# Optimization experiments

Hardware: AMD Instinct MI355X
Metric: run time of the kernel (lower is better)

Reference implementation:

```python
import jax, jax.numpy as jnp
import numpy as np

NUM_HEADS = 16
EMBED_DIM = 1024
HEAD_DIM = EMBED_DIM // NUM_HEADS  # 64
BS, L = 2, 4096


def setup_inputs() -> dict:
    key = jax.random.key(0)
    ks = jax.random.split(key, 11)
    s = 1.0 / np.sqrt(EMBED_DIM)
    inp = {
        "x": jax.random.normal(ks[0], (BS, L, EMBED_DIM), dtype=jnp.float32),
        "mask": jax.random.randint(ks[1], (1, 1, L, L), 0, 2, dtype=jnp.int32),
        # weights stored as [in, out] so y = x @ W + b (math-equivalent to nn.Linear)
        "Wq": jax.random.uniform(ks[2], (EMBED_DIM, EMBED_DIM), jnp.float32, -s, s),
        "bq": jax.random.uniform(ks[3], (EMBED_DIM,), jnp.float32, -s, s),
        "Wk": jax.random.uniform(ks[4], (EMBED_DIM, EMBED_DIM), jnp.float32, -s, s),
        "bk": jax.random.uniform(ks[5], (EMBED_DIM,), jnp.float32, -s, s),
        "Wv": jax.random.uniform(ks[6], (EMBED_DIM, EMBED_DIM), jnp.float32, -s, s),
        "bv": jax.random.uniform(ks[7], (EMBED_DIM,), jnp.float32, -s, s),
        "Wo": jax.random.uniform(ks[8], (EMBED_DIM, EMBED_DIM), jnp.float32, -s, s),
        "bo": jax.random.uniform(ks[9], (EMBED_DIM,), jnp.float32, -s, s),
    }
    return inp


def reference(x, mask, Wq, bq, Wk, bk, Wv, bv, Wo, bo):
    bs, length, _ = x.shape
    scale = jnp.asarray(HEAD_DIM ** 0.5, x.dtype)

    def split_heads(t):  # [b, l, d] -> [b, h, l, hd]
        return t.reshape(bs, length, NUM_HEADS, HEAD_DIM).transpose(0, 2, 1, 3)

    q = split_heads(x @ Wq + bq)
    k = split_heads(x @ Wk + bk)
    v = split_heads(x @ Wv + bv)

    # scores: [b, h, lq, lk]
    scores = jnp.einsum("bhqd,bhkd->bhqk", q, k) / scale
    scores = scores + mask.astype(x.dtype) * jnp.asarray(-10000.0, x.dtype)
    attn = jax.nn.softmax(scores, axis=-1)  # dropout p=0 -> identity

    out = jnp.einsum("bhqk,bhkd->bhqd", attn, v)  # [b, h, l, hd]
    out = out.transpose(0, 2, 1, 3).reshape(bs, length, EMBED_DIM)
    return out @ Wo + bo
```

## Files before the change

### kernel.cpp

```cpp
#include <hip/hip_runtime.h>
#include <stdint.h>

#define SEQ_LEN 4096
#define N_HEADS 16
#define H_DIM 64
#define E_DIM 1024
#define NBH 32
#define M_TOT 8192

typedef __attribute__((ext_vector_type(8))) short short8;
typedef __attribute__((ext_vector_type(4))) short s16x4;
typedef __attribute__((ext_vector_type(4))) float f32x4;
typedef __attribute__((ext_vector_type(4))) unsigned short u16x4;

__device__ __forceinline__ unsigned short f2bf(float f) {
  union { float f; uint32_t u; } c; c.f = f;
  uint32_t u = c.u;
  u += 0x7FFFu + ((u >> 16) & 1u);
  return (unsigned short)(u >> 16);
}

__device__ __forceinline__ f32x4 mfma16(short8 a, short8 b, f32x4 c) {
  return __builtin_amdgcn_mfma_f32_16x16x32_bf16(a, b, c, 0, 0, 0);
}

__device__ __forceinline__ uint32_t cvtpk_bf16(float a, float b) {
  uint32_t r;
  asm("v_cvt_pk_bf16_f32 %0, %1, %2" : "=v"(r) : "v"(a), "v"(b));
  return r;
}

__device__ __forceinline__ float bperm_f(int srcLane, float v) {
  union { float f; int i; } c; c.f = v;
  c.i = __builtin_amdgcn_ds_bpermute(srcLane << 2, c.i);
  return c.f;
}


__global__ __launch_bounds__(256) void cast_x_kernel(const float* __restrict__ x,
                                                     unsigned short* __restrict__ xb) {
  const int i = (blockIdx.x * 256 + threadIdx.x) * 4;
  const f32x4 v = *(const f32x4*)(x + i);
  u16x4 o;
  #pragma unroll
  for (int j = 0; j < 4; j++) o[j] = f2bf(v[j]);
  *(u16x4*)(xb + i) = o;
}

__global__ __launch_bounds__(256) void transpose_w_kernel(
    const float* __restrict__ Wq, const float* __restrict__ Wk,
    const float* __restrict__ Wv, const float* __restrict__ Wo,
    unsigned short* __restrict__ Wqkvt, unsigned short* __restrict__ Wot) {
  __shared__ float tile[32][33];
  const int z = blockIdx.z;
  const float* src = (z == 0) ? Wq : (z == 1) ? Wk : (z == 2) ? Wv : Wo;
  unsigned short* dst = (z < 3) ? (Wqkvt + (size_t)z * E_DIM * E_DIM) : Wot;
  const int n0 = blockIdx.x * 32, k0 = blockIdx.y * 32;
  const int tx = threadIdx.x, ty = threadIdx.y;
  #pragma unroll
  for (int i = 0; i < 4; i++)
    tile[ty + i * 8][tx] = src[(size_t)(k0 + ty + i * 8) * E_DIM + n0 + tx];
  __syncthreads();
  #pragma unroll
  for (int i = 0; i < 4; i++)
    dst[(size_t)(n0 + ty + i * 8) * E_DIM + k0 + tx] = f2bf(tile[tx][ty + i * 8]);
}

__global__ __launch_bounds__(256) void pack_mask_kernel(const int* __restrict__ mask,
                                                        unsigned long long* __restrict__ mw) {
  const int e = blockIdx.x * 256 + threadIdx.x;
  const int bit = mask[e] != 0;
  const unsigned long long bal = __ballot(bit);
  if ((threadIdx.x & 63) == 0) mw[e >> 6] = bal;
}

#define LDT 40
#define QSCALE 0.18033688011112042f

template<int MODE>
__global__ __launch_bounds__(256) void gemm_kernel(
    const unsigned short* __restrict__ A,
    const unsigned short* __restrict__ Bt,
    const float* __restrict__ b0, const float* __restrict__ b1, const float* __restrict__ b2,
    unsigned short* __restrict__ Qo, unsigned short* __restrict__ Ko,
    unsigned short* __restrict__ Vto, float* __restrict__ Co)
{
  __shared__ unsigned short As[128 * LDT];
  __shared__ unsigned short Bs[128 * LDT];
  const int tid = threadIdx.x;
  const int lane = tid & 63, wid = tid >> 6;
  const int l15 = lane & 15, g = lane >> 4;
  const int bm = blockIdx.x * 128, bn = blockIdx.y * 128;
  const int wm = (wid >> 1) * 64, wn = (wid & 1) * 64;

  const int srow = tid >> 2, scol = (tid & 3) * 8;
  const unsigned short* ap0 = A  + (size_t)(bm + srow) * E_DIM + scol;
  const unsigned short* ap1 = ap0 + (size_t)64 * E_DIM;
  const unsigned short* bp0 = Bt + (size_t)(bn + srow) * E_DIM + scol;
  const unsigned short* bp1 = bp0 + (size_t)64 * E_DIM;
  unsigned short* aw0 = As + srow * LDT + scol;
  unsigned short* aw1 = aw0 + 64 * LDT;
  unsigned short* bw0 = Bs + srow * LDT + scol;
  unsigned short* bw1 = bw0 + 64 * LDT;

  f32x4 acc[4][4] = {};

  for (int k0 = 0; k0 < E_DIM; k0 += 32) {
    const short8 ra0 = *(const short8*)(ap0 + k0);
    const short8 ra1 = *(const short8*)(ap1 + k0);
    const short8 rb0 = *(const short8*)(bp0 + k0);
    const short8 rb1 = *(const short8*)(bp1 + k0);
    __syncthreads();
    *(short8*)aw0 = ra0;  *(short8*)aw1 = ra1;
    *(short8*)bw0 = rb0;  *(short8*)bw1 = rb1;
    __syncthreads();
    short8 af[4], bf[4];
    #pragma unroll
    for (int i = 0; i < 4; i++)
      af[i] = *(const short8*)(As + (wm + i * 16 + l15) * LDT + g * 8);
    #pragma unroll
    for (int j = 0; j < 4; j++)
      bf[j] = *(const short8*)(Bs + (wn + j * 16 + l15) * LDT + g * 8);
    #pragma unroll
    for (int i = 0; i < 4; i++)
      #pragma unroll
      for (int j = 0; j < 4; j++)
        acc[i][j] = mfma16(af[i], bf[j], acc[i][j]);
  }

  #pragma unroll
  for (int i = 0; i < 4; i++) {
    #pragma unroll
    for (int j = 0; j < 4; j++) {
      const int n  = bn + wn + j * 16 + l15;
      const int m0 = bm + wm + i * 16 + g * 4;
      if (MODE == 1) {
        const float bias = b0[n];
        #pragma unroll
        for (int r = 0; r < 4; r++)
          Co[(size_t)(m0 + r) * E_DIM + n] = acc[i][j][r] + bias;
      } else {
        const int sec = n >> 10, nn = n & 1023;
        const int h = nn >> 6, d = nn & 63;
        const float bias = (sec == 0 ? b0 : sec == 1 ? b1 : b2)[nn];
        if (sec == 2) {
          u16x4 vv;
          #pragma unroll
          for (int r = 0; r < 4; r++) vv[r] = f2bf(acc[i][j][r] + bias);
          const int b = m0 >> 12, l0 = m0 & 4095;
          *(u16x4*)(Vto + ((size_t)(b * N_HEADS + h) * H_DIM + d) * SEQ_LEN + l0) = vv;
        } else {
          unsigned short* dst = (sec == 0) ? Qo : Ko;
          const float scl = (sec == 0) ? QSCALE : 1.0f;
          #pragma unroll
          for (int r = 0; r < 4; r++) {
            const int m = m0 + r;
            const int b = m >> 12, l = m & 4095;
            dst[((size_t)(b * N_HEADS + h) * SEQ_LEN + l) * H_DIM + d] =
                f2bf((acc[i][j][r] + bias) * scl);
          }
        }
      }
    }
  }
}

#define LDK 72
#define LDV 136
#define DEFER_THR 8.0f

__global__ __launch_bounds__(256, 2) void attn_kernel(
    const unsigned short* __restrict__ Qg, const unsigned short* __restrict__ Kg,
    const unsigned short* __restrict__ Vg, const unsigned long long* __restrict__ mw,
    unsigned short* __restrict__ Ob)
{
  __shared__ unsigned short Ks[128 * LDK];
  __shared__ unsigned short Vs[64 * LDV];
  const int tid = threadIdx.x, lane = tid & 63, wid = tid >> 6;
  const int l15 = lane & 15, g = lane >> 4;
  const int q0 = blockIdx.x * 128, bh = blockIdx.y;
  const unsigned short* Qp = Qg + ((size_t)bh * SEQ_LEN + q0 + wid * 32) * H_DIM;
  const unsigned short* Kp = Kg + (size_t)bh * SEQ_LEN * H_DIM;
  const unsigned short* Vp = Vg + (size_t)bh * H_DIM * SEQ_LEN;

  short8 qf[2][2];
  #pragma unroll
  for (int i = 0; i < 2; i++)
    #pragma unroll
    for (int h = 0; h < 2; h++)
      qf[i][h] = *(const short8*)(Qp + (i * 16 + l15) * H_DIM + h * 32 + g * 8);

  float m_run[2] = {-1e30f, -1e30f}, l_run[2] = {0.f, 0.f};
  f32x4 acc[2][4] = {};

  for (int kt = 0; kt < SEQ_LEN / 128; kt++) {
    short8 rk[4], rv[4];
    #pragma unroll
    for (int it = 0; it < 4; it++) {
      const int idx = it * 256 + tid;
      rk[it] = *(const short8*)(Kp + (size_t)(kt * 128 + (idx >> 3)) * H_DIM + (idx & 7) * 8);
      rv[it] = *(const short8*)(Vp + (size_t)(idx >> 4) * SEQ_LEN + kt * 128 + (idx & 15) * 8);
    }
    __syncthreads();
    #pragma unroll
    for (int it = 0; it < 4; it++) {
      const int idx = it * 256 + tid;
      *(short8*)(Ks + (idx >> 3) * LDK + (idx & 7) * 8) = rk[it];
      const int d = idx >> 4, c = (idx & 15) * 8;
      const int base1 = (c >> 5) * 32 + ((c & 15) >> 2) * 8 + ((c >> 4) & 1) * 4;
      s16x4 lo, hi;
      #pragma unroll
      for (int e = 0; e < 4; e++) { lo[e] = rv[it][e]; hi[e] = rv[it][e + 4]; }
      *(s16x4*)(Vs + d * LDV + base1) = lo;
      *(s16x4*)(Vs + d * LDV + base1 + 8) = hi;
    }
    __syncthreads();

    f32x4 s[2][8];
    #pragma unroll
    for (int j = 0; j < 8; j++) {
      const short8 kf0 = *(const short8*)(Ks + (j * 16 + l15) * LDK + g * 8);
      const short8 kf1 = *(const short8*)(Ks + (j * 16 + l15) * LDK + 32 + g * 8);
      #pragma unroll
      for (int i = 0; i < 2; i++) {
        f32x4 z = {0.f, 0.f, 0.f, 0.f};
        z = mfma16(kf0, qf[i][0], z);
        s[i][j] = mfma16(kf1, qf[i][1], z);
      }
    }

    unsigned long long wsh0[2], wsh1[2];
    #pragma unroll
    for (int i = 0; i < 2; i++) {
      const unsigned long long* mp =
          mw + (size_t)(q0 + wid * 32 + i * 16 + l15) * (SEQ_LEN / 64) + kt * 2;
      wsh0[i] = mp[0] >> (g * 4);
      wsh1[i] = mp[1] >> (g * 4);
    }

    float tm[2];
    #pragma unroll
    for (int i = 0; i < 2; i++) {
      f32x4 t4 = s[i][0];
      #pragma unroll
      for (int j = 1; j < 8; j++)
        #pragma unroll
        for (int r = 0; r < 4; r++) t4[r] = fmaxf(t4[r], s[i][j][r]);
      float t = fmaxf(fmaxf(t4[0], t4[1]), fmaxf(t4[2], t4[3]));
      t = fmaxf(t, __shfl_xor(t, 16));
      t = fmaxf(t, __shfl_xor(t, 32));
      tm[i] = t;
    }

    const int need = (tm[0] > m_run[0] + DEFER_THR) | (tm[1] > m_run[1] + DEFER_THR);
    if (__any(need)) {
      #pragma unroll
      for (int i = 0; i < 2; i++) {
        const float mn = fmaxf(m_run[i], tm[i]);
        const float corr = __builtin_amdgcn_exp2f(m_run[i] - mn);
        m_run[i] = mn;
        l_run[i] *= corr;
        float cR[4];
        #pragma unroll
        for (int r = 0; r < 4; r++) cR[r] = bperm_f(g * 4 + r, corr);
        #pragma unroll
        for (int dsub = 0; dsub < 4; dsub++)
          #pragma unroll
          for (int r = 0; r < 4; r++) acc[i][dsub][r] *= cR[r];
      }
    }

    #pragma unroll
    for (int i = 0; i < 2; i++) {
      f32x4 sum4 = {0.f, 0.f, 0.f, 0.f};
      #pragma unroll
      for (int j = 0; j < 8; j++) {
        const unsigned long long w = (j < 4) ? wsh0[i] : wsh1[i];
        #pragma unroll
        for (int r = 0; r < 4; r++) {
          const float p = __builtin_amdgcn_exp2f(s[i][j][r] - m_run[i]);
          const uint32_t bit = (uint32_t)(w >> ((j & 3) * 16 + r)) & 1u;
          s[i][j][r] = __uint_as_float(__float_as_uint(p) & (bit - 1u));
        }
        #pragma unroll
        for (int r = 0; r < 4; r++) sum4[r] += s[i][j][r];
      }
      float rs = (sum4[0] + sum4[1]) + (sum4[2] + sum4[3]);
      rs += __shfl_xor(rs, 16);
      rs += __shfl_xor(rs, 32);
      l_run[i] += rs;
    }

    #pragma unroll
    for (int kk = 0; kk < 4; kk++) {
      union { short8 s8; uint32_t u[4]; } pa0, pa1;
      pa0.u[0] = cvtpk_bf16(s[0][2 * kk][0], s[0][2 * kk][1]);
      pa0.u[1] = cvtpk_bf16(s[0][2 * kk][2], s[0][2 * kk][3]);
      pa0.u[2] = cvtpk_bf16(s[0][2 * kk + 1][0], s[0][2 * kk + 1][1]);
      pa0.u[3] = cvtpk_bf16(s[0][2 * kk + 1][2], s[0][2 * kk + 1][3]);
      pa1.u[0] = cvtpk_bf16(s[1][2 * kk][0], s[1][2 * kk][1]);
      pa1.u[1] = cvtpk_bf16(s[1][2 * kk][2], s[1][2 * kk][3]);
      pa1.u[2] = cvtpk_bf16(s[1][2 * kk + 1][0], s[1][2 * kk + 1][1]);
      pa1.u[3] = cvtpk_bf16(s[1][2 * kk + 1][2], s[1][2 * kk + 1][3]);
      #pragma unroll
      for (int dsub = 0; dsub < 4; dsub++) {
        const short8 vf = *(const short8*)(Vs + (dsub * 16 + l15) * LDV + kk * 32 + g * 8);
        acc[0][dsub] = mfma16(pa0.s8, vf, acc[0][dsub]);
        acc[1][dsub] = mfma16(pa1.s8, vf, acc[1][dsub]);
      }
    }
  }

  const int b = bh >> 4, h = bh & 15;
  #pragma unroll
  for (int i = 0; i < 2; i++) {
    float inv[4];
    #pragma unroll
    for (int r = 0; r < 4; r++) inv[r] = 1.f / bperm_f(g * 4 + r, l_run[i]);
    #pragma unroll
    for (int dsub = 0; dsub < 4; dsub++)
      #pragma unroll
      for (int r = 0; r < 4; r++) {
        const int qrow = q0 + wid * 32 + i * 16 + g * 4 + r;
        Ob[((size_t)b * SEQ_LEN + qrow) * E_DIM + h * H_DIM + dsub * 16 + l15] =
            f2bf(acc[i][dsub][r] * inv[r]);
      }
  }
}

extern "C" void kernel_launch(void* const* d_in, const int* in_sizes, int n_in,
                              void* d_out, int out_size, void* d_ws, size_t ws_size,
                              hipStream_t stream) {
  const float* x  = (const float*)d_in[0];
  const int* mask = (const int*)d_in[1];
  const float* Wq = (const float*)d_in[2];
  const float* bq = (const float*)d_in[3];
  const float* Wk = (const float*)d_in[4];
  const float* bk = (const float*)d_in[5];
  const float* Wv = (const float*)d_in[6];
  const float* bv = (const float*)d_in[7];
  const float* Wo = (const float*)d_in[8];
  const float* bo = (const float*)d_in[9];

  char* ws = (char*)d_ws;
  unsigned short* xb     = (unsigned short*)(ws);
  unsigned short* Wqkvt  = (unsigned short*)(ws + ((size_t)16 << 20));
  unsigned short* Wot    = (unsigned short*)(ws + ((size_t)22 << 20));
  unsigned short* Qb     = (unsigned short*)(ws + ((size_t)24 << 20));
  unsigned short* Kb     = (unsigned short*)(ws + ((size_t)40 << 20));
  unsigned short* Vtb    = (unsigned short*)(ws + ((size_t)56 << 20));
  unsigned long long* mw = (unsigned long long*)(ws + ((size_t)72 << 20));
  unsigned short* Ob = xb;

  cast_x_kernel<<<8192, 256, 0, stream>>>(x, xb);
  transpose_w_kernel<<<dim3(32, 32, 4), dim3(32, 8), 0, stream>>>(Wq, Wk, Wv, Wo, Wqkvt, Wot);
  pack_mask_kernel<<<65536, 256, 0, stream>>>(mask, mw);
  gemm_kernel<0><<<dim3(64, 24), 256, 0, stream>>>(xb, Wqkvt, bq, bk, bv, Qb, Kb, Vtb, nullptr);
  attn_kernel<<<dim3(32, 32), 256, 0, stream>>>(Qb, Kb, Vtb, mw, Ob);
  gemm_kernel<1><<<dim3(64, 8), 256, 0, stream>>>(Ob, Wot, bo, nullptr, nullptr,
                                                  nullptr, nullptr, nullptr, (float*)d_out);
}
```

Baseline: 507.5 us.

## Double-buffer LDS in GEMM and attention, compute softmax row sums via MFMA

Both the projection GEMM and the attention kernel now use two LDS buffers. The next tile's global loads are issued before computing on the current tile, which leaves one barrier per iteration instead of two. The attention kernel also remaps block indices to spread heads across the grid, and it starts the running max at a fixed value of 4 instead of -1e30. It replaces the shuffle-based row-sum reduction with an extra MFMA against a vector of ones. The costs are doubled LDS use, more register pressure, and a row sum taken from bf16-rounded probabilities, which could lower occupancy or shift accuracy slightly.

```diff
diff --git a/kernel.cpp b/kernel.cpp
--- a/kernel.cpp
+++ b/kernel.cpp
@@ -7,6 +7,7 @@
 #define E_DIM 1024
 #define NBH 32
 #define M_TOT 8192
+#define KTILES (SEQ_LEN / 128)
 
 typedef __attribute__((ext_vector_type(8))) short short8;
 typedef __attribute__((ext_vector_type(4))) short s16x4;
@@ -85,8 +86,8 @@
     unsigned short* __restrict__ Qo, unsigned short* __restrict__ Ko,
     unsigned short* __restrict__ Vto, float* __restrict__ Co)
 {
-  __shared__ unsigned short As[128 * LDT];
-  __shared__ unsigned short Bs[128 * LDT];
+  __shared__ unsigned short As[2][128 * LDT];
+  __shared__ unsigned short Bs[2][128 * LDT];
   const int tid = threadIdx.x;
   const int lane = tid & 63, wid = tid >> 6;
   const int l15 = lane & 15, g = lane >> 4;
@@ -98,34 +99,49 @@
   const unsigned short* ap1 = ap0 + (size_t)64 * E_DIM;
   const unsigned short* bp0 = Bt + (size_t)(bn + srow) * E_DIM + scol;
   const unsigned short* bp1 = bp0 + (size_t)64 * E_DIM;
-  unsigned short* aw0 = As + srow * LDT + scol;
-  unsigned short* aw1 = aw0 + 64 * LDT;
-  unsigned short* bw0 = Bs + srow * LDT + scol;
-  unsigned short* bw1 = bw0 + 64 * LDT;
+  const int w0 = srow * LDT + scol, w1 = w0 + 64 * LDT;
 
   f32x4 acc[4][4] = {};
 
+  short8 ra0 = *(const short8*)(ap0);
+  short8 ra1 = *(const short8*)(ap1);
+  short8 rb0 = *(const short8*)(bp0);
+  short8 rb1 = *(const short8*)(bp1);
+  *(short8*)(&As[0][0] + w0) = ra0;  *(short8*)(&As[0][0] + w1) = ra1;
+  *(short8*)(&Bs[0][0] + w0) = rb0;  *(short8*)(&Bs[0][0] + w1) = rb1;
+  __syncthreads();
+
+  int cur = 0;
   for (int k0 = 0; k0 < E_DIM; k0 += 32) {
-    const short8 ra0 = *(const short8*)(ap0 + k0);
-    const short8 ra1 = *(const short8*)(ap1 + k0);
-    const short8 rb0 = *(const short8*)(bp0 + k0);
-    const short8 rb1 = *(const short8*)(bp1 + k0);
-    __syncthreads();
-    *(short8*)aw0 = ra0;  *(short8*)aw1 = ra1;
-    *(short8*)bw0 = rb0;  *(short8*)bw1 = rb1;
-    __syncthreads();
+    const bool hasn = (k0 + 32) < E_DIM;
+    if (hasn) {
+      ra0 = *(const short8*)(ap0 + k0 + 32);
+      ra1 = *(const short8*)(ap1 + k0 + 32);
+      rb0 = *(const short8*)(bp0 + k0 + 32);
+      rb1 = *(const short8*)(bp1 + k0 + 32);
+    }
+    const unsigned short* AsC = &As[cur][0];
+    const unsigned short* BsC = &Bs[cur][0];
     short8 af[4], bf[4];
     #pragma unroll
     for (int i = 0; i < 4; i++)
-      af[i] = *(const short8*)(As + (wm + i * 16 + l15) * LDT + g * 8);
+      af[i] = *(const short8*)(AsC + (wm + i * 16 + l15) * LDT + g * 8);
     #pragma unroll
     for (int j = 0; j < 4; j++)
-      bf[j] = *(const short8*)(Bs + (wn + j * 16 + l15) * LDT + g * 8);
+      bf[j] = *(const short8*)(BsC + (wn + j * 16 + l15) * LDT + g * 8);
     #pragma unroll
     for (int i = 0; i < 4; i++)
       #pragma unroll
       for (int j = 0; j < 4; j++)
         acc[i][j] = mfma16(af[i], bf[j], acc[i][j]);
+    if (hasn) {
+      unsigned short* AsN = &As[cur ^ 1][0];
+      unsigned short* BsN = &Bs[cur ^ 1][0];
+      *(short8*)(AsN + w0) = ra0;  *(short8*)(AsN + w1) = ra1;
+      *(short8*)(BsN + w0) = rb0;  *(short8*)(BsN + w1) = rb1;
+    }
+    __syncthreads();
+    cur ^= 1;
   }
 
   #pragma unroll
@@ -174,11 +190,13 @@
     const unsigned short* __restrict__ Vg, const unsigned long long* __restrict__ mw,
     unsigned short* __restrict__ Ob)
 {
-  __shared__ unsigned short Ks[128 * LDK];
-  __shared__ unsigned short Vs[64 * LDV];
+  __shared__ unsigned short Ks[2][128 * LDK];
+  __shared__ unsigned short Vs[2][64 * LDV];
   const int tid = threadIdx.x, lane = tid & 63, wid = tid >> 6;
   const int l15 = lane & 15, g = lane >> 4;
-  const int q0 = blockIdx.x * 128, bh = blockIdx.y;
+  const int p = blockIdx.y * 32 + blockIdx.x;
+  const int L = (p & 7) * 128 + (p >> 3);
+  const int q0 = (L & 31) * 128, bh = L >> 5;
   const unsigned short* Qp = Qg + ((size_t)bh * SEQ_LEN + q0 + wid * 32) * H_DIM;
   const unsigned short* Kp = Kg + (size_t)bh * SEQ_LEN * H_DIM;
   const unsigned short* Vp = Vg + (size_t)bh * H_DIM * SEQ_LEN;
@@ -190,37 +208,76 @@
     for (int h = 0; h < 2; h++)
       qf[i][h] = *(const short8*)(Qp + (i * 16 + l15) * H_DIM + h * 32 + g * 8);
 
-  float m_run[2] = {-1e30f, -1e30f}, l_run[2] = {0.f, 0.f};
+  const unsigned short* kg[4];
+  const unsigned short* vg[4];
+  int kw[4], vw[4];
+  #pragma unroll
+  for (int it = 0; it < 4; it++) {
+    const int idx = it * 256 + tid;
+    const int rk_ = idx >> 3, ck_ = (idx & 7) * 8;
+    const int rv_ = idx >> 4, cv_ = (idx & 15) * 8;
+    const int b1 = (cv_ >> 5) * 32 + ((cv_ & 15) >> 2) * 8 + ((cv_ >> 4) & 1) * 4;
+    kg[it] = Kp + (size_t)rk_ * H_DIM + ck_;
+    vg[it] = Vp + (size_t)rv_ * SEQ_LEN + cv_;
+    kw[it] = rk_ * LDK + ck_;
+    vw[it] = rv_ * LDV + b1;
+  }
+  const unsigned long long* mbase[2];
+  #pragma unroll
+  for (int i = 0; i < 2; i++)
+    mbase[i] = mw + (size_t)(q0 + wid * 32 + i * 16 + l15) * (SEQ_LEN / 64);
+
+  float m_run[2] = {4.0f, 4.0f};
   f32x4 acc[2][4] = {};
-
-  for (int kt = 0; kt < SEQ_LEN / 128; kt++) {
-    short8 rk[4], rv[4];
-    #pragma unroll
-    for (int it = 0; it < 4; it++) {
-      const int idx = it * 256 + tid;
-      rk[it] = *(const short8*)(Kp + (size_t)(kt * 128 + (idx >> 3)) * H_DIM + (idx & 7) * 8);
-      rv[it] = *(const short8*)(Vp + (size_t)(idx >> 4) * SEQ_LEN + kt * 128 + (idx & 15) * 8);
-    }
-    __syncthreads();
-    #pragma unroll
-    for (int it = 0; it < 4; it++) {
-      const int idx = it * 256 + tid;
-      *(short8*)(Ks + (idx >> 3) * LDK + (idx & 7) * 8) = rk[it];
-      const int d = idx >> 4, c = (idx & 15) * 8;
-      const int base1 = (c >> 5) * 32 + ((c & 15) >> 2) * 8 + ((c >> 4) & 1) * 4;
-      s16x4 lo, hi;
-      #pragma unroll
-      for (int e = 0; e < 4; e++) { lo[e] = rv[it][e]; hi[e] = rv[it][e + 4]; }
-      *(s16x4*)(Vs + d * LDV + base1) = lo;
-      *(s16x4*)(Vs + d * LDV + base1 + 8) = hi;
-    }
-    __syncthreads();
+  f32x4 accl[2] = {};
+  const short8 vone = {(short)0x3F80, (short)0x3F80, (short)0x3F80, (short)0x3F80,
+                       (short)0x3F80, (short)0x3F80, (short)0x3F80, (short)0x3F80};
+
+  short8 rk[4], rv[4];
+  #pragma unroll
+  for (int it = 0; it < 4; it++) {
+    rk[it] = *(const short8*)(kg[it]);
+    rv[it] = *(const short8*)(vg[it]);
+  }
+  #pragma unroll
+  for (int it = 0; it < 4; it++) {
+    *(short8*)(&Ks[0][0] + kw[it]) = rk[it];
+    s16x4 lo, hi;
+    #pragma unroll
+    for (int e = 0; e < 4; e++) { lo[e] = rv[it][e]; hi[e] = rv[it][e + 4]; }
+    *(s16x4*)(&Vs[0][0] + vw[it]) = lo;
+    *(s16x4*)(&Vs[0][0] + vw[it] + 8) = hi;
+  }
+  __syncthreads();
+
+  int cur = 0;
+  for (int kt = 0; kt < KTILES; kt++) {
+    const bool hasn = (kt + 1) < KTILES;
+    if (hasn) {
+      #pragma unroll
+      for (int it = 0; it < 4; it++) {
+        rk[it] = *(const short8*)(kg[it] + (size_t)(kt + 1) * 128 * H_DIM);
+        rv[it] = *(const short8*)(vg[it] + (kt + 1) * 128);
+      }
+    }
+    unsigned long long wA[2], wB[2];
+    #pragma unroll
+    for (int i = 0; i < 2; i++) {
+      const unsigned long long* mp = mbase[i] + kt * 2;
+      wA[i] = mp[0] >> (g * 4);
+      wB[i] = mp[1] >> (g * 4);
+    }
+
+    const unsigned short* KsC = &Ks[cur][0];
+    const unsigned short* VsC = &Vs[cur][0];
+    unsigned short* KsN = &Ks[cur ^ 1][0];
+    unsigned short* VsN = &Vs[cur ^ 1][0];
 
     f32x4 s[2][8];
     #pragma unroll
     for (int j = 0; j < 8; j++) {
-      const short8 kf0 = *(const short8*)(Ks + (j * 16 + l15) * LDK + g * 8);
-      const short8 kf1 = *(const short8*)(Ks + (j * 16 + l15) * LDK + 32 + g * 8);
+      const short8 kf0 = *(const short8*)(KsC + (j * 16 + l15) * LDK + g * 8);
+      const short8 kf1 = *(const short8*)(KsC + (j * 16 + l15) * LDK + 32 + g * 8);
       #pragma unroll
       for (int i = 0; i < 2; i++) {
         f32x4 z = {0.f, 0.f, 0.f, 0.f};
@@ -229,66 +286,73 @@
       }
     }
 
-    unsigned long long wsh0[2], wsh1[2];
+    if (hasn) {
+      #pragma unroll
+      for (int it = 0; it < 4; it++) *(short8*)(KsN + kw[it]) = rk[it];
+    }
+
+    float tm[2];
     #pragma unroll
     for (int i = 0; i < 2; i++) {
-      const unsigned long long* mp =
-          mw + (size_t)(q0 + wid * 32 + i * 16 + l15) * (SEQ_LEN / 64) + kt * 2;
-      wsh0[i] = mp[0] >> (g * 4);
-      wsh1[i] = mp[1] >> (g * 4);
-    }
-
-    float tm[2];
-    #pragma unroll
-    for (int i = 0; i < 2; i++) {
-      f32x4 t4 = s[i][0];
-      #pragma unroll
-      for (int j = 1; j < 8; j++)
-        #pragma unroll
-        for (int r = 0; r < 4; r++) t4[r] = fmaxf(t4[r], s[i][j][r]);
+      f32x4 t4;
+      #pragma unroll
+      for (int r = 0; r < 4; r++) {
+        const float a = fmaxf(fmaxf(s[i][0][r], s[i][1][r]), s[i][2][r]);
+        const float b = fmaxf(fmaxf(s[i][3][r], s[i][4][r]), s[i][5][r]);
+        const float c = fmaxf(fmaxf(a, s[i][6][r]), s[i][7][r]);
+        t4[r] = fmaxf(b, c);
+      }
       float t = fmaxf(fmaxf(t4[0], t4[1]), fmaxf(t4[2], t4[3]));
       t = fmaxf(t, __shfl_xor(t, 16));
       t = fmaxf(t, __shfl_xor(t, 32));
       tm[i] = t;
     }
 
-    const int need = (tm[0] > m_run[0] + DEFER_THR) | (tm[1] > m_run[1] + DEFER_THR);
-    if (__any(need)) {
+    if (__any((tm[0] > m_run[0] + DEFER_THR) | (tm[1] > m_run[1] + DEFER_THR))) {
       #pragma unroll
       for (int i = 0; i < 2; i++) {
         const float mn = fmaxf(m_run[i], tm[i]);
         const float corr = __builtin_amdgcn_exp2f(m_run[i] - mn);
         m_run[i] = mn;
-        l_run[i] *= corr;
         float cR[4];
         #pragma unroll
         for (int r = 0; r < 4; r++) cR[r] = bperm_f(g * 4 + r, corr);
         #pragma unroll
-        for (int dsub = 0; dsub < 4; dsub++)
+        for (int r = 0; r < 4; r++) accl[i][r] *= cR[r];
+        #pragma unroll
+        for (int d = 0; d < 4; d++)
           #pragma unroll
-          for (int r = 0; r < 4; r++) acc[i][dsub][r] *= cR[r];
+          for (int r = 0; r < 4; r++) acc[i][d][r] *= cR[r];
       }
     }
 
     #pragma unroll
     for (int i = 0; i < 2; i++) {
-      f32x4 sum4 = {0.f, 0.f, 0.f, 0.f};
+      const uint32_t a0 = (uint32_t)wA[i], a1 = (uint32_t)(wA[i] >> 32);
+      const uint32_t b0 = (uint32_t)wB[i], b1 = (uint32_t)(wB[i] >> 32);
       #pragma unroll
       for (int j = 0; j < 8; j++) {
-        const unsigned long long w = (j < 4) ? wsh0[i] : wsh1[i];
         #pragma unroll
         for (int r = 0; r < 4; r++) {
-          const float p = __builtin_amdgcn_exp2f(s[i][j][r] - m_run[i]);
-          const uint32_t bit = (uint32_t)(w >> ((j & 3) * 16 + r)) & 1u;
-          s[i][j][r] = __uint_as_float(__float_as_uint(p) & (bit - 1u));
+          const int idx = (j & 3) * 16 + r;
+          const uint32_t word = (j < 4) ? ((idx < 32) ? a0 : a1)
+                                        : ((idx < 32) ? b0 : b1);
+          const uint32_t bit = (word >> (idx & 31)) & 1u;
+          const float pf = __builtin_amdgcn_exp2f(s[i][j][r] - m_run[i]);
+          s[i][j][r] = __uint_as_float(__float_as_uint(pf) & (bit - 1u));
         }
-        #pragma unroll
-        for (int r = 0; r < 4; r++) sum4[r] += s[i][j][r];
-      }
-      float rs = (sum4[0] + sum4[1]) + (sum4[2] + sum4[3]);
-      rs += __shfl_xor(rs, 16);
-      rs += __shfl_xor(rs, 32);
-      l_run[i] += rs;
+      }
+    }
+
+    if (hasn) {
+      #pragma unroll
+      for (int it = 0; it < 4; it++) {
+        s16x4 lo, hi;
+        #pragma unroll
+        for (int e = 0; e < 4; e++) { lo[e] = rv[it][e]; hi[e] = rv[it][e + 4]; }
+        *(s16x4*)(VsN + vw[it]) = lo;
+        *(s16x4*)(VsN + vw[it] + 8) = hi;
+      }
     }
 
     #pragma unroll
@@ -302,13 +366,18 @@
       pa1.u[1] = cvtpk_bf16(s[1][2 * kk][2], s[1][2 * kk][3]);
       pa1.u[2] = cvtpk_bf16(s[1][2 * kk + 1][0], s[1][2 * kk + 1][1]);
       pa1.u[3] = cvtpk_bf16(s[1][2 * kk + 1][2], s[1][2 * kk + 1][3]);
+      accl[0] = mfma16(pa0.s8, vone, accl[0]);
+      accl[1] = mfma16(pa1.s8, vone, accl[1]);
       #pragma unroll
       for (int dsub = 0; dsub < 4; dsub++) {
-        const short8 vf = *(const short8*)(Vs + (dsub * 16 + l15) * LDV + kk * 32 + g * 8);
+        const short8 vf = *(const short8*)(VsC + (dsub * 16 + l15) * LDV + kk * 32 + g * 8);
         acc[0][dsub] = mfma16(pa0.s8, vf, acc[0][dsub]);
         acc[1][dsub] = mfma16(pa1.s8, vf, acc[1][dsub]);
       }
     }
+
+    __syncthreads();
+    cur ^= 1;
   }
 
   const int b = bh >> 4, h = bh & 15;
@@ -316,7 +385,7 @@
   for (int i = 0; i < 2; i++) {
     float inv[4];
     #pragma unroll
-    for (int r = 0; r < 4; r++) inv[r] = 1.f / bperm_f(g * 4 + r, l_run[i]);
+    for (int r = 0; r < 4; r++) inv[r] = 1.f / accl[i][r];
     #pragma unroll
     for (int dsub = 0; dsub < 4; dsub++)
       #pragma unroll
```

Result: faster. 473.8 us (-6.6%).
